# Optimization experiments

Hardware: AMD Instinct MI355X
Metric: run time of the kernel (lower is better)

The kernel has to match this reference:

```python
import jax, jax.numpy as jnp
import numpy as np

C = 128  # n_atom_basis


def setup_inputs() -> dict:
    key = jax.random.key(0)
    k_h, k_A, k_Ww, k_Wb, k_aw, k_ab = jax.random.split(key, 6)
    B, N = 8, 2048
    h = jax.random.normal(k_h, (B, N, C), dtype=jnp.float32)
    A = jax.random.uniform(k_A, (B, N, N), dtype=jnp.float32)
    # nn.Linear(C, C)
    lim_W = 1.0 / np.sqrt(C)
    W_w = jax.random.uniform(k_Ww, (C, C), minval=-lim_W, maxval=lim_W, dtype=jnp.float32)
    W_b = jax.random.uniform(k_Wb, (C,), minval=-lim_W, maxval=lim_W, dtype=jnp.float32)
    # nn.Linear(2C, 1)
    lim_a = 1.0 / np.sqrt(2 * C)
    a_w = jax.random.uniform(k_aw, (2 * C,), minval=-lim_a, maxval=lim_a, dtype=jnp.float32)
    a_b = jax.random.uniform(k_ab, (), minval=-lim_a, maxval=lim_a, dtype=jnp.float32)
    return {"h": h, "A": A, "W_w": W_w, "W_b": W_b, "a_w": a_w, "a_b": a_b}


def reference(h, A, W_w, W_b, a_w, a_b):
    # Wh computed once ([B,N,C]) instead of the original's redundant [B,N,N,C] broadcast.
    Wh = jnp.einsum('bnc,dc->bnd', h, W_w) + W_b
    # a([hi, hj]) = a_w[:C]@Wh_i + a_w[C:]@Wh_j + a_b  -> rank-1 decomposition of the concat-linear
    si = Wh @ a_w[:C]          # [B,N]
    sj = Wh @ a_w[C:]          # [B,N]
    s = si[:, :, None] + sj[:, None, :] + a_b  # [B,N,N] raw scores
    e = jnp.exp(s) * A                          # masked exp (no max-subtraction: matches original math)
    alpha = e / jnp.sum(e, axis=2, keepdims=True)
    # weighted sum over neighbors j of the ORIGINAL h (as in the source, not Wh)
    h_prime = jnp.einsum('bij,bjc->bic', alpha, h)
    return h_prime
```

## Files before the change

kernel.cpp:

```cpp
#include <hip/hip_runtime.h>
#include <math.h>
#include <stdint.h>

#define Bn 8
#define Nn 2048
#define Cn 128

typedef _Float16 f16x8 __attribute__((ext_vector_type(8)));
typedef float    f32x4 __attribute__((ext_vector_type(4)));

__global__ void prep_kernel(const float* __restrict__ Ww, const float* __restrict__ Wb,
                            const float* __restrict__ aw, float* __restrict__ vout) {
    int c = threadIdx.x;
    float acc = 0.f;
    for (int d = 0; d < Cn; ++d) acc += Ww[d * Cn + c] * aw[Cn + d];
    vout[c] = acc;
    if (c == 0) {
        float b2 = 0.f;
        for (int i = 0; i < Cn; ++i) b2 += Wb[i] * aw[Cn + i];
        vout[Cn] = b2;
    }
}

__global__ __launch_bounds__(256) void rows_kernel(const float* __restrict__ h,
                                                   const float* __restrict__ vb2,
                                                   float* __restrict__ wexp,
                                                   _Float16* __restrict__ hT) {
    __shared__ float tile[64][133];
    int bid = blockIdx.x;
    int b   = bid >> 5;
    int n0  = (bid & 31) << 6;
    const float* hblk = h + ((size_t)(b * Nn + n0)) * Cn;
    int tid = threadIdx.x;

    {
        int r = tid >> 2, qq = tid & 3;
        const float4* rowp = (const float4*)(hblk + (size_t)r * Cn);
#pragma unroll
        for (int i = 0; i < 8; ++i) {
            int f4 = i * 4 + qq;
            float4 x = rowp[f4];
            int cb = f4 * 4;
            tile[r][cb + 0] = x.x; tile[r][cb + 1] = x.y;
            tile[r][cb + 2] = x.z; tile[r][cb + 3] = x.w;
        }
    }
    __syncthreads();

    if (tid < 64) {
        float acc = 0.f;
        for (int i = 0; i < Cn; ++i) acc += tile[tid][i] * vb2[i];
        wexp[b * Nn + n0 + tid] = expf(acc + vb2[Cn]);
    }

    int lane = tid & 63, cg = tid >> 6;
    for (int c = cg; c < Cn; c += 4) {
        hT[((size_t)(b * Cn + c)) * Nn + n0 + lane] = (_Float16)tile[lane][c];
    }
}

__global__ __launch_bounds__(512) void attn_kernel(const float* __restrict__ A,
                                                   const float* __restrict__ wexp,
                                                   const _Float16* __restrict__ hT,
                                                   float* __restrict__ out) {
    __shared__ float red[64 * 132];
    __shared__ float dred[64];

    int bid = blockIdx.x;
    int b   = bid >> 5;
    int i0  = (bid & 31) << 6;
    int tid = threadIdx.x;
    int w = tid >> 6, l = tid & 63;
    int rw = w & 3, k2 = w >> 2;
    int m = l & 15, q = l >> 4;
    int row_l = rw * 16 + m;

    const float*    Arow = A    + ((size_t)(b * Nn + i0 + row_l)) * Nn;
    const float*    wb   = wexp + (size_t)b * Nn;
    const _Float16* hTb  = hT   + (size_t)b * Cn * Nn;

    f32x4 acc[8];
#pragma unroll
    for (int t = 0; t < 8; ++t) acc[t] = (f32x4){0.f, 0.f, 0.f, 0.f};
    float dsum = 0.f;

    for (int t = 0; t < 32; ++t) {
        int j = k2 * 32 + t * 64 + q * 8;
        float4 a0 = *(const float4*)(Arow + j);
        float4 a1 = *(const float4*)(Arow + j + 4);
        float4 w0 = *(const float4*)(wb + j);
        float4 w1 = *(const float4*)(wb + j + 4);
        float p0 = a0.x * w0.x, p1 = a0.y * w0.y, p2 = a0.z * w0.z, p3 = a0.w * w0.w;
        float p4 = a1.x * w1.x, p5 = a1.y * w1.y, p6 = a1.z * w1.z, p7 = a1.w * w1.w;
        dsum += ((p0 + p1) + (p2 + p3)) + ((p4 + p5) + (p6 + p7));
        f16x8 af;
        af[0] = (_Float16)p0; af[1] = (_Float16)p1; af[2] = (_Float16)p2; af[3] = (_Float16)p3;
        af[4] = (_Float16)p4; af[5] = (_Float16)p5; af[6] = (_Float16)p6; af[7] = (_Float16)p7;
        const _Float16* hcol = hTb + j;
#pragma unroll
        for (int tt = 0; tt < 8; ++tt) {
            f16x8 bf = *(const f16x8*)(hcol + (size_t)(tt * 16 + m) * Nn);
            acc[tt] = __builtin_amdgcn_mfma_f32_16x16x32_f16(af, bf, acc[tt], 0, 0, 0);
        }
    }

    dsum += __shfl_xor(dsum, 16, 64);
    dsum += __shfl_xor(dsum, 32, 64);

    if (k2 == 1) {
        if (l < 16) dred[row_l] = dsum;
#pragma unroll
        for (int tt = 0; tt < 8; ++tt)
#pragma unroll
            for (int r = 0; r < 4; ++r)
                red[(rw * 16 + q * 4 + r) * 132 + tt * 16 + m] = acc[tt][r];
    }
    __syncthreads();
    if (k2 == 0) {
        float dtot = dsum + dred[row_l];
        float invd = 1.f / dtot;
        float* ob = out + ((size_t)(b * Nn + i0)) * Cn;
#pragma unroll
        for (int r = 0; r < 4; ++r) {
            int rloc = q * 4 + r;
            float iv = __shfl(invd, rloc, 64);
#pragma unroll
            for (int tt = 0; tt < 8; ++tt) {
                float v = (acc[tt][r] + red[(rw * 16 + rloc) * 132 + tt * 16 + m]) * iv;
                ob[(size_t)(rw * 16 + rloc) * Cn + tt * 16 + m] = v;
            }
        }
    }
}

extern "C" void kernel_launch(void* const* d_in, const int* in_sizes, int n_in,
                              void* d_out, int out_size, void* d_ws, size_t ws_size,
                              hipStream_t stream) {
    const float* h  = (const float*)d_in[0];
    const float* A  = (const float*)d_in[1];
    const float* Ww = (const float*)d_in[2];
    const float* Wb = (const float*)d_in[3];
    const float* aw = (const float*)d_in[4];
    float* out = (float*)d_out;

    char* ws = (char*)d_ws;
    _Float16* hT   = (_Float16*)ws;
    float*    wexp = (float*)(ws + (size_t)Bn * Cn * Nn * 2);
    float*    vout = (float*)(ws + (size_t)Bn * Cn * Nn * 2 + (size_t)Bn * Nn * 4);

    prep_kernel<<<1, 128, 0, stream>>>(Ww, Wb, aw, vout);
    rows_kernel<<<Bn * (Nn / 64), 256, 0, stream>>>(h, vout, wexp, hT);
    attn_kernel<<<Bn * (Nn / 64), 512, 0, stream>>>(A, wexp, hT, out);
}
```

Measured before the change: 256.7 us.

## Fuse prep into rows kernel, tile hT by k-blocks, split attn over 4 k-waves

Removes the separate single-block prep kernel by having every rows block recompute the W·a projection vector redundantly. The transposed fp16 h is stored in 32-wide k-blocks so each MFMA B-fragment load is contiguous instead of strided by N. The attention kernel now handles 32 rows per block with 4-way k-splitting, doubling the grid for better occupancy, and B fragments are prefetched before the A loads. It also interleaves batch in the block index. The cost is redundant Ww reads per block and a larger cross-wave reduction through shared memory.

```diff
diff --git a/kernel.cpp b/kernel.cpp
--- a/kernel.cpp
+++ b/kernel.cpp
@@ -5,129 +5,159 @@
 #define Bn 8
 #define Nn 2048
 #define Cn 128
+#define NKB (Nn / 32)
 
 typedef _Float16 f16x8 __attribute__((ext_vector_type(8)));
 typedef float    f32x4 __attribute__((ext_vector_type(4)));
 
-__global__ void prep_kernel(const float* __restrict__ Ww, const float* __restrict__ Wb,
-                            const float* __restrict__ aw, float* __restrict__ vout) {
-    int c = threadIdx.x;
-    float acc = 0.f;
-    for (int d = 0; d < Cn; ++d) acc += Ww[d * Cn + c] * aw[Cn + d];
-    vout[c] = acc;
-    if (c == 0) {
-        float b2 = 0.f;
-        for (int i = 0; i < Cn; ++i) b2 += Wb[i] * aw[Cn + i];
-        vout[Cn] = b2;
-    }
-}
+__global__ __launch_bounds__(256) void rows_kernel(const float* __restrict__ h,
+                                                   const float* __restrict__ Ww,
+                                                   const float* __restrict__ Wb,
+                                                   const float* __restrict__ aw,
+                                                   float* __restrict__ wexp,
+                                                   _Float16* __restrict__ hTt) {
+    __shared__ float tile[64][132];
+    __shared__ float vsh[128];
+    __shared__ float vpart[128];
+    __shared__ float b2sh;
 
-__global__ __launch_bounds__(256) void rows_kernel(const float* __restrict__ h,
-                                                   const float* __restrict__ vb2,
-                                                   float* __restrict__ wexp,
-                                                   _Float16* __restrict__ hT) {
-    __shared__ float tile[64][133];
     int bid = blockIdx.x;
-    int b   = bid >> 5;
-    int n0  = (bid & 31) << 6;
-    const float* hblk = h + ((size_t)(b * Nn + n0)) * Cn;
+    int b   = bid & 7;
+    int n0  = (bid >> 3) << 6;
     int tid = threadIdx.x;
 
     {
+        int c = tid & 127, half = tid >> 7;
+        float acc = 0.f;
+#pragma unroll
+        for (int dd = 0; dd < 64; ++dd) {
+            int d = half * 64 + dd;
+            acc += Ww[d * Cn + c] * aw[Cn + d];
+        }
+        if (half) vpart[c] = acc; else vsh[c] = acc;
+    }
+    if (tid < 64) {
+        float b2p = Wb[tid] * aw[Cn + tid] + Wb[tid + 64] * aw[Cn + tid + 64];
+        b2p += __shfl_xor(b2p, 32, 64);
+        b2p += __shfl_xor(b2p, 16, 64);
+        b2p += __shfl_xor(b2p, 8, 64);
+        b2p += __shfl_xor(b2p, 4, 64);
+        b2p += __shfl_xor(b2p, 2, 64);
+        b2p += __shfl_xor(b2p, 1, 64);
+        if (tid == 0) b2sh = b2p;
+    }
+    {
         int r = tid >> 2, qq = tid & 3;
-        const float4* rowp = (const float4*)(hblk + (size_t)r * Cn);
+        const float4* rowp = (const float4*)(h + (size_t)(b * Nn + n0 + r) * Cn);
 #pragma unroll
         for (int i = 0; i < 8; ++i) {
             int f4 = i * 4 + qq;
             float4 x = rowp[f4];
-            int cb = f4 * 4;
-            tile[r][cb + 0] = x.x; tile[r][cb + 1] = x.y;
-            tile[r][cb + 2] = x.z; tile[r][cb + 3] = x.w;
+            *(float4*)&tile[r][f4 * 4] = x;
         }
     }
     __syncthreads();
 
-    if (tid < 64) {
+    {
+        int r = tid >> 2, pp = tid & 3;
         float acc = 0.f;
-        for (int i = 0; i < Cn; ++i) acc += tile[tid][i] * vb2[i];
-        wexp[b * Nn + n0 + tid] = expf(acc + vb2[Cn]);
+#pragma unroll
+        for (int ii = 0; ii < 32; ++ii) {
+            int i = pp * 32 + ii;
+            acc += tile[r][i] * (vsh[i] + vpart[i]);
+        }
+        acc += __shfl_xor(acc, 1, 64);
+        acc += __shfl_xor(acc, 2, 64);
+        if (pp == 0) wexp[b * Nn + n0 + r] = expf(acc + b2sh);
     }
 
-    int lane = tid & 63, cg = tid >> 6;
-    for (int c = cg; c < Cn; c += 4) {
-        hT[((size_t)(b * Cn + c)) * Nn + n0 + lane] = (_Float16)tile[lane][c];
+    {
+        int l = tid & 63, cg = tid >> 6;
+        int kb = (n0 >> 5) + (l >> 5);
+        int ks = l & 31;
+        _Float16* base = hTt + ((size_t)(b * NKB + kb) * Cn) * 32 + ks;
+#pragma unroll
+        for (int c = cg; c < Cn; c += 4)
+            base[c * 32] = (_Float16)tile[l][c];
     }
 }
 
-__global__ __launch_bounds__(512) void attn_kernel(const float* __restrict__ A,
-                                                   const float* __restrict__ wexp,
-                                                   const _Float16* __restrict__ hT,
-                                                   float* __restrict__ out) {
-    __shared__ float red[64 * 132];
-    __shared__ float dred[64];
+__global__ __launch_bounds__(512, 4) void attn_kernel(const float* __restrict__ A,
+                                                      const float* __restrict__ wexp,
+                                                      const _Float16* __restrict__ hTt,
+                                                      float* __restrict__ out) {
+    __shared__ float red[3][32][132];
+    __shared__ float dred[3][32];
 
     int bid = blockIdx.x;
-    int b   = bid >> 5;
-    int i0  = (bid & 31) << 6;
+    int b   = bid & 7;
+    int i0  = (bid >> 3) << 5;
     int tid = threadIdx.x;
     int w = tid >> 6, l = tid & 63;
-    int rw = w & 3, k2 = w >> 2;
+    int rw = w & 1, kw = w >> 1;
     int m = l & 15, q = l >> 4;
     int row_l = rw * 16 + m;
 
-    const float*    Arow = A    + ((size_t)(b * Nn + i0 + row_l)) * Nn;
+    const float*    Arow = A    + (size_t)(b * Nn + i0 + row_l) * Nn;
     const float*    wb   = wexp + (size_t)b * Nn;
-    const _Float16* hTb  = hT   + (size_t)b * Cn * Nn;
+    const _Float16* hb   = hTt  + (size_t)b * NKB * Cn * 32;
 
     f32x4 acc[8];
 #pragma unroll
     for (int t = 0; t < 8; ++t) acc[t] = (f32x4){0.f, 0.f, 0.f, 0.f};
     float dsum = 0.f;
 
-    for (int t = 0; t < 32; ++t) {
-        int j = k2 * 32 + t * 64 + q * 8;
+    for (int t = 0; t < 16; ++t) {
+        int kb = kw + t * 4;
+        int j  = kb * 32 + q * 8;
+        const _Float16* hk = hb + (size_t)kb * (Cn * 32) + q * 8;
+        f16x8 bfv[8];
+#pragma unroll
+        for (int tt = 0; tt < 8; ++tt)
+            bfv[tt] = *(const f16x8*)(hk + (tt * 16 + m) * 32);
         float4 a0 = *(const float4*)(Arow + j);
         float4 a1 = *(const float4*)(Arow + j + 4);
         float4 w0 = *(const float4*)(wb + j);
         float4 w1 = *(const float4*)(wb + j + 4);
+
         float p0 = a0.x * w0.x, p1 = a0.y * w0.y, p2 = a0.z * w0.z, p3 = a0.w * w0.w;
         float p4 = a1.x * w1.x, p5 = a1.y * w1.y, p6 = a1.z * w1.z, p7 = a1.w * w1.w;
         dsum += ((p0 + p1) + (p2 + p3)) + ((p4 + p5) + (p6 + p7));
         f16x8 af;
         af[0] = (_Float16)p0; af[1] = (_Float16)p1; af[2] = (_Float16)p2; af[3] = (_Float16)p3;
         af[4] = (_Float16)p4; af[5] = (_Float16)p5; af[6] = (_Float16)p6; af[7] = (_Float16)p7;
-        const _Float16* hcol = hTb + j;
 #pragma unroll
-        for (int tt = 0; tt < 8; ++tt) {
-            f16x8 bf = *(const f16x8*)(hcol + (size_t)(tt * 16 + m) * Nn);
-            acc[tt] = __builtin_amdgcn_mfma_f32_16x16x32_f16(af, bf, acc[tt], 0, 0, 0);
-        }
+        for (int tt = 0; tt < 8; ++tt)
+            acc[tt] = __builtin_amdgcn_mfma_f32_16x16x32_f16(af, bfv[tt], acc[tt], 0, 0, 0);
     }
 
     dsum += __shfl_xor(dsum, 16, 64);
     dsum += __shfl_xor(dsum, 32, 64);
 
-    if (k2 == 1) {
-        if (l < 16) dred[row_l] = dsum;
+    if (kw > 0) {
+        if (l < 16) dred[kw - 1][row_l] = dsum;
 #pragma unroll
         for (int tt = 0; tt < 8; ++tt)
 #pragma unroll
             for (int r = 0; r < 4; ++r)
-                red[(rw * 16 + q * 4 + r) * 132 + tt * 16 + m] = acc[tt][r];
+                red[kw - 1][rw * 16 + q * 4 + r][tt * 16 + m] = acc[tt][r];
     }
     __syncthreads();
-    if (k2 == 0) {
-        float dtot = dsum + dred[row_l];
+    if (kw == 0) {
+        float dtot = dsum + dred[0][row_l] + dred[1][row_l] + dred[2][row_l];
         float invd = 1.f / dtot;
-        float* ob = out + ((size_t)(b * Nn + i0)) * Cn;
+        float* ob = out + (size_t)(b * Nn + i0 + rw * 16) * Cn;
 #pragma unroll
         for (int r = 0; r < 4; ++r) {
             int rloc = q * 4 + r;
             float iv = __shfl(invd, rloc, 64);
 #pragma unroll
             for (int tt = 0; tt < 8; ++tt) {
-                float v = (acc[tt][r] + red[(rw * 16 + rloc) * 132 + tt * 16 + m]) * iv;
-                ob[(size_t)(rw * 16 + rloc) * Cn + tt * 16 + m] = v;
+                int cc = tt * 16 + m;
+                float v = acc[tt][r] + red[0][rw * 16 + rloc][cc]
+                                     + red[1][rw * 16 + rloc][cc]
+                                     + red[2][rw * 16 + rloc][cc];
+                ob[(size_t)rloc * Cn + cc] = v * iv;
             }
         }
     }
@@ -144,11 +174,9 @@
     float* out = (float*)d_out;
 
     char* ws = (char*)d_ws;
-    _Float16* hT   = (_Float16*)ws;
-    float*    wexp = (float*)(ws + (size_t)Bn * Cn * Nn * 2);
-    float*    vout = (float*)(ws + (size_t)Bn * Cn * Nn * 2 + (size_t)Bn * Nn * 4);
+    _Float16* hTt  = (_Float16*)ws;
+    float*    wexp = (float*)(ws + (size_t)Bn * NKB * Cn * 32 * 2);
 
-    prep_kernel<<<1, 128, 0, stream>>>(Ww, Wb, aw, vout);
-    rows_kernel<<<Bn * (Nn / 64), 256, 0, stream>>>(h, vout, wexp, hT);
-    attn_kernel<<<Bn * (Nn / 64), 512, 0, stream>>>(A, wexp, hT, out);
+    rows_kernel<<<Bn * (Nn / 64), 256, 0, stream>>>(h, Ww, Wb, aw, wexp, hTt);
+    attn_kernel<<<Bn * (Nn / 32), 512, 0, stream>>>(A, wexp, hTt, out);
 }
```

Result: faster. 234.9 us (-8.5%).
